# Kernel optimization log

Measured on AMD Instinct MI355X. Metric: run time of the kernel, lower is better.

## Reference

```python
import jax, jax.numpy as jnp
import numpy as np

IMG_DIM = 28 * 28


def _distmat(X):
    # D[i,j] = ||x_i||^2 - 2 x_i.x_j + ||x_j||^2
    r = jnp.sum(X * X, axis=1)
    a = X @ X.T
    return r[:, None] - 2.0 * a + r[None, :]


def _sigma_from_self(D, m):
    """Replicates sigma_estimation(X, X): median of the strict lower triangle of
    distmat(cat([X, X])), which is the 2x2 block-tiled matrix [[D,D],[D,D]].
    Its strict lower triangle multiset = full D (block 2,1) + 2x strict tril(D).
    Clamps: if med<=0 use mean; floor at 0.01. Detached (stop_gradient), matching
    the torch .detach().cpu().numpy() path."""
    mask = jnp.tril(jnp.ones((m, m), dtype=bool), -1)
    tril_inf = jnp.where(mask, D, jnp.inf)
    vals = jnp.concatenate([D.ravel(), tril_inf.ravel(), tril_inf.ravel()])
    s = jnp.sort(vals)  # inf padding sorts to the end
    k = 2 * m * m - m  # number of strict-lower-triangle entries of a 2m x 2m matrix
    if k % 2 == 0:
        med = 0.5 * (s[k // 2 - 1] + s[k // 2])  # np.median averages middles
    else:
        med = s[(k - 1) // 2]
    tri_sum = jnp.sum(jnp.where(mask, D, 0.0))
    mean_tri = (jnp.sum(D) + 2.0 * tri_sum) / k
    med = jnp.where(med <= 0.0, mean_tri, med)
    med = jnp.maximum(med, 0.01)
    return jax.lax.stop_gradient(med)


def _centered_kernel(D, sigma):
    # Kxc = Kx @ (I - ones/m)  ==  Kx - rowmean(Kx)
    K = jnp.exp(-D / (2.0 * sigma * sigma))
    return K - jnp.mean(K, axis=1, keepdims=True)


def _hsic_norm_from_kernels(Kxc, Kyc):
    Pxy = jnp.mean(Kxc * Kyc.T)
    Px = jnp.sqrt(jnp.mean(Kxc * Kxc.T))
    Py = jnp.sqrt(jnp.mean(Kyc * Kyc.T))
    return Pxy / (Px * Py)


def reference(x, y):
    x2 = x.reshape((-1, IMG_DIM))  # [m, 784]
    m = x2.shape[0]
    d = y.shape[-1]

    # hsic_normalized(x, y) with per-variable median sigma
    Dx = _distmat(x2)
    Dy = _distmat(y)
    Kx = _centered_kernel(Dx, _sigma_from_self(Dx, m))
    Ky = _centered_kernel(Dy, _sigma_from_self(Dy, m))
    mi_io = _hsic_norm_from_kernels(Kx, Ky)

    # Batched version of the nested loop over latent component pairs (i<j).
    # Per-column 1-D distance matrices: [d, m, m]
    yt = y.T  # [d, m]
    Dc = (yt[:, :, None] - yt[:, None, :]) ** 2
    sig = jax.vmap(lambda D: _sigma_from_self(D, m))(Dc)  # [d]
    Kc = jnp.exp(-Dc / (2.0 * sig * sig)[:, None, None])
    Kc = Kc - jnp.mean(Kc, axis=2, keepdims=True)  # centered, [d, m, m]

    # P[a,b] = mean(K_a * K_b^T)
    P = jnp.einsum('aij,bji->ab', Kc, Kc) / (m * m)
    diag = jnp.diagonal(P)
    norm = P / jnp.sqrt(diag[:, None] * diag[None, :])
    pair_mask = jnp.triu(jnp.ones((d, d), dtype=bool), 1)  # i < j
    mi_component_sum = jnp.sum(jnp.where(pair_mask, norm, 0.0))

    return -mi_io + mi_component_sum


def setup_inputs() -> dict:
    key = jax.random.key(0)
    kx, ky = jax.random.split(key)
    x = jax.random.normal(kx, (2048, 784), dtype=jnp.float32)
    y = jax.random.normal(ky, (2048, 10), dtype=jnp.float32)
    return {"x": x, "y": y}
```

## Files before the change

### kernel.cpp

```cpp
#include <hip/hip_runtime.h>
#include <math.h>

constexpr int Md   = 2048;
constexpr int NDIM = 784;
constexpr int DYC  = 10;
constexpr int MM   = Md * Md;
constexpr unsigned RANK_LO = 4193279u;
constexpr unsigned RANK_HI = 4193280u;
constexpr int NPROB = 12;
constexpr int NB    = 256;
constexpr int NBINS = 8192;

constexpr size_t OFF_DX     = 0;
constexpr size_t OFF_DY     = OFF_DX + (size_t)MM * 4;
constexpr size_t OFF_RX     = OFF_DY + (size_t)MM * 4;
constexpr size_t OFF_RY     = OFF_RX + Md * 8;
constexpr size_t OFF_RC     = OFF_RY + Md * 8;
constexpr size_t OFF_GACC   = OFF_RC + (size_t)DYC * Md * 8;
constexpr size_t OFF_HISTA  = OFF_GACC + 64 * 8;
constexpr size_t OFF_HISTB  = OFF_HISTA + (size_t)NPROB * NBINS * 4;
constexpr size_t OFF_RES    = OFF_HISTB + (size_t)NPROB * NBINS * 4;
constexpr size_t OFF_JOBS   = OFF_RES + 72 * 8;
constexpr size_t OFF_Q      = OFF_JOBS + NPROB * 5 * 4;
constexpr size_t OFF_RXN    = OFF_Q + NPROB * 4;
constexpr size_t OFF_YT     = OFF_RXN + Md * 4;
constexpr size_t WS_NEED    = OFF_YT + (size_t)DYC * Md * 4;
constexpr size_t ZERO_BASE  = OFF_GACC;
constexpr size_t ZERO_LEN   = OFF_JOBS - OFF_GACC;

typedef _Float16 f16x8 __attribute__((ext_vector_type(8)));
typedef _Float16 f16x4 __attribute__((ext_vector_type(4)));
typedef float    f32x16 __attribute__((ext_vector_type(16)));

__device__ __forceinline__ unsigned fkey(float v) {
  unsigned u = __float_as_uint(v);
  return (u & 0x80000000u) ? ~u : (u | 0x80000000u);
}
__device__ __forceinline__ float keyinv(unsigned k) {
  unsigned u = (k & 0x80000000u) ? (k ^ 0x80000000u) : ~k;
  return __uint_as_float(u);
}
__device__ __forceinline__ f16x8 ld8(const _Float16* p) {
  f16x4 lo = *(const f16x4*)p;
  f16x4 hi = *(const f16x4*)(p + 4);
  f16x8 r;
  r[0]=lo[0]; r[1]=lo[1]; r[2]=lo[2]; r[3]=lo[3];
  r[4]=hi[0]; r[5]=hi[1]; r[6]=hi[2]; r[7]=hi[3];
  return r;
}
__device__ __forceinline__ double waveReduceD(double v) {
  #pragma unroll
  for (int o = 32; o > 0; o >>= 1) v += __shfl_down(v, o, 64);
  return v;
}
__device__ __forceinline__ double blockReduceD(double v) {
  __shared__ double sred[4];
  v = waveReduceD(v);
  int lane = threadIdx.x & 63;
  int w    = threadIdx.x >> 6;
  __syncthreads();
  if (lane == 0) sred[w] = v;
  __syncthreads();
  double r = 0.0;
  if (threadIdx.x == 0) { r = sred[0] + sred[1] + sred[2] + sred[3]; }
  return r;
}

__global__ void fail_kernel(float* out) { if (threadIdx.x == 0) out[0] = 0.0f; }

__global__ __launch_bounds__(256) void prep_kernel(const float* __restrict__ X,
                                                   const float* __restrict__ Y,
                                                   float* __restrict__ rxn,
                                                   float* __restrict__ Yt,
                                                   unsigned* __restrict__ jobs) {
  int bb = blockIdx.x;
  if (bb < Md) {
    double acc = 0.0;
    for (int k = threadIdx.x; k < NDIM; k += 256) {
      float v = X[bb * NDIM + k];
      acc += (double)v * (double)v;
    }
    double r = blockReduceD(acc);
    if (threadIdx.x == 0) rxn[bb] = (float)r;
  } else if (bb < Md + 80) {
    int e = (bb - Md) * 256 + threadIdx.x;
    if (e < Md * DYC) {
      int i = e / DYC, c = e % DYC;
      Yt[c * Md + i] = Y[e];
    }
  } else {
    int t = threadIdx.x;
    if (t < NPROB * 5) {
      int w = t % 5;
      jobs[t] = (w == 1) ? RANK_LO : (w == 3) ? RANK_HI : 0u;
    }
  }
}

__global__ __launch_bounds__(256) void dist_kernel(const float* __restrict__ X,
                                                   const float* __restrict__ Y,
                                                   const float* __restrict__ rxn,
                                                   float* __restrict__ Dx,
                                                   float* __restrict__ Dy) {
  __shared__ _Float16 Ah[64][68], Al[64][68], Bh[64][68], Bl[64][68];
  __shared__ float Yi[64][10], Yj[64][10];
  const int tid = threadIdx.x;
  const int i0 = blockIdx.y * 64, j0 = blockIdx.x * 64;

  if (blockIdx.z == 1) {
    for (int t = tid; t < 640; t += 256) {
      int r = t / 10, c = t % 10;
      Yi[r][c] = Y[(i0 + r) * DYC + c];
      Yj[r][c] = Y[(j0 + r) * DYC + c];
    }
    __syncthreads();
    int jj = tid & 63;
    int ii0 = (tid >> 6) * 16;
    float yj[10];
    #pragma unroll
    for (int c = 0; c < 10; ++c) yj[c] = Yj[jj][c];
    for (int r = 0; r < 16; ++r) {
      int ii = ii0 + r;
      float s = 0.f;
      #pragma unroll
      for (int c = 0; c < 10; ++c) { float d = Yi[ii][c] - yj[c]; s = fmaf(d, d, s); }
      Dy[(size_t)(i0 + ii) * Md + (j0 + jj)] = s;
    }
    return;
  }

  const int wave = tid >> 6, lane = tid & 63;
  const int wr = (wave >> 1) * 32, wc = (wave & 1) * 32;
  const int srow = tid >> 2;
  const int sseg = (tid & 3) * 8;

  f32x16 acc_hh = {}, acc_c1 = {}, acc_c2 = {};

  const float* Arow = X + (size_t)(i0 + srow) * NDIM;
  const float* Brow = X + (size_t)(j0 + srow) * NDIM;
  const int lrow = lane & 31;
  const int lko  = (lane >> 5) * 8;

  for (int k0 = 0; k0 < 800; k0 += 32) {
    float a[8], b[8];
    if (k0 + 32 <= NDIM) {
      float4 a4 = *(const float4*)(Arow + k0 + sseg);
      float4 a5 = *(const float4*)(Arow + k0 + sseg + 4);
      float4 b4 = *(const float4*)(Brow + k0 + sseg);
      float4 b5 = *(const float4*)(Brow + k0 + sseg + 4);
      a[0]=a4.x; a[1]=a4.y; a[2]=a4.z; a[3]=a4.w; a[4]=a5.x; a[5]=a5.y; a[6]=a5.z; a[7]=a5.w;
      b[0]=b4.x; b[1]=b4.y; b[2]=b4.z; b[3]=b4.w; b[4]=b5.x; b[5]=b5.y; b[6]=b5.z; b[7]=b5.w;
    } else {
      #pragma unroll
      for (int u = 0; u < 8; ++u) {
        int k = k0 + sseg + u;
        a[u] = (k < NDIM) ? Arow[k] : 0.0f;
        b[u] = (k < NDIM) ? Brow[k] : 0.0f;
      }
    }
    __syncthreads();
    #pragma unroll
    for (int half = 0; half < 2; ++half) {
      f16x4 vah, val_, vbh, vbl;
      #pragma unroll
      for (int u = 0; u < 4; ++u) {
        float av = a[half * 4 + u];
        _Float16 h = (_Float16)av;
        vah[u] = h; val_[u] = (_Float16)(av - (float)h);
        float bv = b[half * 4 + u];
        _Float16 g = (_Float16)bv;
        vbh[u] = g; vbl[u] = (_Float16)(bv - (float)g);
      }
      *(f16x4*)&Ah[srow][sseg + half * 4] = vah;
      *(f16x4*)&Al[srow][sseg + half * 4] = val_;
      *(f16x4*)&Bh[srow][sseg + half * 4] = vbh;
      *(f16x4*)&Bl[srow][sseg + half * 4] = vbl;
    }
    __syncthreads();
    #pragma unroll
    for (int ks = 0; ks < 2; ++ks) {
      int ko = ks * 16 + lko;
      f16x8 fah = ld8(&Ah[wr + lrow][ko]);
      f16x8 fal = ld8(&Al[wr + lrow][ko]);
      f16x8 fbh = ld8(&Bh[wc + lrow][ko]);
      f16x8 fbl = ld8(&Bl[wc + lrow][ko]);
      acc_hh = __builtin_amdgcn_mfma_f32_32x32x16_f16(fah, fbh, acc_hh, 0, 0, 0);
      acc_c1 = __builtin_amdgcn_mfma_f32_32x32x16_f16(fah, fbl, acc_c1, 0, 0, 0);
      acc_c2 = __builtin_amdgcn_mfma_f32_32x32x16_f16(fal, fbh, acc_c2, 0, 0, 0);
    }
  }
  int col = j0 + wc + (lane & 31);
  float rj = rxn[col];
  #pragma unroll
  for (int r = 0; r < 16; ++r) {
    int row = i0 + wr + (r & 3) + 8 * (r >> 2) + 4 * (lane >> 5);
    float t = rxn[row] + rj;
    float cc = acc_c1[r] + acc_c2[r];
    Dx[(size_t)row * Md + col] = fmaf(-2.0f, cc, fmaf(-2.0f, acc_hh[r], t));
  }
}

__global__ __launch_bounds__(256) void hist_kernel(const float* __restrict__ Dx,
                                                   const float* __restrict__ Dy,
                                                   const float* __restrict__ Yt,
                                                   unsigned* __restrict__ histA,
                                                   unsigned* __restrict__ histB,
                                                   const unsigned* __restrict__ jobs,
                                                   int level) {
  __shared__ unsigned lh[NBINS];
  __shared__ float ycol[Md];
  int prob = blockIdx.y;
  for (int b = threadIdx.x; b < NBINS; b += 256) lh[b] = 0;
  const float* Mptr = (prob == 0) ? Dx : (prob == 1 ? Dy : nullptr);
  if (prob >= 2) {
    const float* src = Yt + (size_t)(prob - 2) * Md;
    for (int i = threadIdx.x; i < Md; i += 256) ycol[i] = src[i];
  }
  __syncthreads();
  unsigned pfxL = jobs[prob * 5 + 0];
  unsigned pfxH = jobs[prob * 5 + 2];
  unsigned div  = jobs[prob * 5 + 4];
  unsigned* ghB = histB + prob * NBINS;

  auto histo = [&](float v, unsigned w) {
    unsigned key = fkey(v);
    if (level == 0) {
      atomicAdd(&lh[key >> 19], w);
    } else if (level == 1) {
      if ((key >> 19) == pfxL)             atomicAdd(&lh[(key >> 6) & 8191u], w);
      else if (div && (key >> 19) == pfxH) atomicAdd(&ghB[(key >> 6) & 8191u], w);
    } else {
      if ((key >> 6) == pfxL)              atomicAdd(&lh[key & 63u], w);
      else if (div && (key >> 6) == pfxH)  atomicAdd(&ghB[key & 63u], w);
    }
  };

  for (int r = 0; r < Md / NB; ++r) {
    int i = blockIdx.x + r * NB;
    int n = i + 1, ng = n >> 2, tail = n & 3;
    if (Mptr) {
      const float4* row4 = (const float4*)(Mptr + (size_t)i * Md);
      for (int g = threadIdx.x; g < ng; g += 256) {
        float4 v = row4[g];
        int jb = g << 2;
        histo(v.x, (jb == i) ? 1u : 4u);
        histo(v.y, (jb + 1 == i) ? 1u : 4u);
        histo(v.z, (jb + 2 == i) ? 1u : 4u);
        histo(v.w, (jb + 3 == i) ? 1u : 4u);
      }
      if (threadIdx.x < tail) {
        int j = (ng << 2) + threadIdx.x;
        histo(Mptr[(size_t)i * Md + j], (j == i) ? 1u : 4u);
      }
    } else {
      float yi = ycol[i];
      for (int g = threadIdx.x; g < ng; g += 256) {
        float4 y4 = *(const float4*)&ycol[g << 2];
        int jb = g << 2;
        float d0 = yi - y4.x, d1 = yi - y4.y, d2 = yi - y4.z, d3 = yi - y4.w;
        histo(d0 * d0, (jb == i) ? 1u : 4u);
        histo(d1 * d1, (jb + 1 == i) ? 1u : 4u);
        histo(d2 * d2, (jb + 2 == i) ? 1u : 4u);
        histo(d3 * d3, (jb + 3 == i) ? 1u : 4u);
      }
      if (threadIdx.x < tail) {
        int j = (ng << 2) + threadIdx.x;
        float d = yi - ycol[j];
        histo(d * d, (j == i) ? 1u : 4u);
      }
    }
  }
  __syncthreads();
  unsigned* ghA = histA + prob * NBINS;
  for (int b = threadIdx.x; b < NBINS; b += 256) {
    unsigned v = lh[b];
    if (v) atomicAdd(&ghA[b], v);
  }
}

__global__ __launch_bounds__(256) void select_kernel(unsigned* __restrict__ histA,
                                                     unsigned* __restrict__ histB,
                                                     unsigned* __restrict__ jobs,
                                                     float* __restrict__ q,
                                                     int level) {
  __shared__ unsigned lhA[NBINS], lhB[NBINS];
  __shared__ unsigned psA[256], psB[256];
  int prob = blockIdx.x;
  int nbins = (level == 2) ? 64 : NBINS;
  int C = (nbins + 255) / 256;
  unsigned* ghA = histA + prob * NBINS;
  unsigned* ghB = histB + prob * NBINS;
  unsigned sA = 0, sB = 0;
  for (int k = 0; k < C; ++k) {
    int b = threadIdx.x * C + k;
    if (b < nbins) {
      unsigned v = ghA[b]; lhA[b] = v; sA += v;
      unsigned u = ghB[b]; lhB[b] = u; sB += u;
    }
  }
  psA[threadIdx.x] = sA; psB[threadIdx.x] = sB;
  __syncthreads();
  if (threadIdx.x == 0) {
    unsigned pfxL = jobs[prob * 5 + 0], remL = jobs[prob * 5 + 1];
    unsigned pfxH = jobs[prob * 5 + 2], remH = jobs[prob * 5 + 3];
    unsigned wasdiv = jobs[prob * 5 + 4];

    auto scan = [&](const unsigned* ps, const unsigned* lhp, unsigned r,
                    int& bin, unsigned& cum) {
      unsigned c = 0; int t = 0;
      for (; t < 255; ++t) { if (c + ps[t] > r) break; c += ps[t]; }
      int b = t * C;
      int be = b + C - 1; if (be > nbins - 1) be = nbins - 1;
      for (; b < be; ++b) { if (c + lhp[b] > r) break; c += lhp[b]; }
      bin = b; cum = c;
    };

    int bL; unsigned cL; scan(psA, lhA, remL, bL, cL);
    int bH; unsigned cH;
    unsigned div = wasdiv;
    if (!wasdiv) {
      scan(psA, lhA, remH, bH, cH);
      if (bH != bL) div = 1;
    } else {
      scan(psB, lhB, remH, bH, cH);
    }
    unsigned baseH = wasdiv ? pfxH : pfxL;
    if (level < 2) {
      jobs[prob * 5 + 0] = (level == 0) ? (unsigned)bL : ((pfxL << 13) | (unsigned)bL);
      jobs[prob * 5 + 2] = (level == 0) ? (unsigned)bH : ((baseH << 13) | (unsigned)bH);
      jobs[prob * 5 + 1] = remL - cL;
      jobs[prob * 5 + 3] = remH - cH;
      jobs[prob * 5 + 4] = div;
    } else {
      unsigned keyL = (pfxL << 6) | (unsigned)bL;
      unsigned keyH = (baseH << 6) | (unsigned)bH;
      float med = 0.5f * (keyinv(keyL) + keyinv(keyH));
      med = fmaxf(med, 0.01f);
      q[prob] = 2.0f * med * med;
    }
  }
  __syncthreads();
  for (int b = threadIdx.x; b < nbins; b += 256) { ghA[b] = 0; ghB[b] = 0; }
}

__global__ __launch_bounds__(256, 4) void phase3_kernel(const float* __restrict__ Dx,
                                                        const float* __restrict__ Dy,
                                                        const float* __restrict__ Yt,
                                                        const float* __restrict__ q,
                                                        double* __restrict__ Rx,
                                                        double* __restrict__ Ry,
                                                        double* __restrict__ Rc,
                                                        double* __restrict__ gacc) {
  __shared__ double shred[224];
  const int wave = threadIdx.x >> 6, lane = threadIdx.x & 63;
  int bb = blockIdx.x;

  if (bb < 256) {
    const float qx = q[0], qy = q[1];
    double gxx = 0, gxy = 0, gyy = 0;
    #pragma unroll
    for (int rr = 0; rr < 2; ++rr) {
      int i = bb * 4 + wave + rr * 1024;
      const float4* rx4 = (const float4*)(Dx + (size_t)i * Md);
      const float4* ry4 = (const float4*)(Dy + (size_t)i * Md);
      double ax = 0, ay = 0;
      #pragma unroll
      for (int it = 0; it < 8; ++it) {
        float4 xv = rx4[it * 64 + lane];
        float4 yv = ry4[it * 64 + lane];
        #pragma unroll
        for (int u = 0; u < 4; ++u) {
          float xe = (u == 0) ? xv.x : (u == 1) ? xv.y : (u == 2) ? xv.z : xv.w;
          float ye = (u == 0) ? yv.x : (u == 1) ? yv.y : (u == 2) ? yv.z : yv.w;
          float ex = expm1f(-(xe / qx));
          float ey = expm1f(-(ye / qy));
          ax += (double)ex; ay += (double)ey;
          gxx += (double)ex * ex;
          gxy += (double)ex * ey;
          gyy += (double)ey * ey;
        }
      }
      ax = waveReduceD(ax);
      ay = waveReduceD(ay);
      if (lane == 0) { Rx[i] = ax; Ry[i] = ay; }
    }
    gxx = waveReduceD(gxx);
    gxy = waveReduceD(gxy);
    gyy = waveReduceD(gyy);
    if (lane == 0) { shred[wave] = gxx; shred[4 + wave] = gxy; shred[8 + wave] = gyy; }
    __syncthreads();
    if (threadIdx.x == 0) {
      atomicAdd(&gacc[0], shred[0] + shred[1] + shred[2] + shred[3]);
      atomicAdd(&gacc[1], shred[4] + shred[5] + shred[6] + shred[7]);
      atomicAdd(&gacc[2], shred[8] + shred[9] + shred[10] + shred[11]);
    }
  } else if (bb < 768) {
    int i = (bb - 256) * 4 + wave;
    float yi[10], ninv[10];
    #pragma unroll
    for (int c = 0; c < 10; ++c) { yi[c] = Yt[c * Md + i]; ninv[c] = -1.0f / q[2 + c]; }
    float facc[10] = {};
    #pragma unroll 2
    for (int it = 0; it < 8; ++it) {
      int j = it * 256 + lane * 4;
      #pragma unroll
      for (int c = 0; c < 10; ++c) {
        float4 v = *(const float4*)(Yt + c * Md + j);
        float d0 = yi[c] - v.x, d1 = yi[c] - v.y, d2 = yi[c] - v.z, d3 = yi[c] - v.w;
        facc[c] += __expf(d0 * d0 * ninv[c]) - 1.0f;
        facc[c] += __expf(d1 * d1 * ninv[c]) - 1.0f;
        facc[c] += __expf(d2 * d2 * ninv[c]) - 1.0f;
        facc[c] += __expf(d3 * d3 * ninv[c]) - 1.0f;
      }
    }
    #pragma unroll
    for (int c = 0; c < 10; ++c) {
      double r = waveReduceD((double)facc[c]);
      if (lane == 0) Rc[c * Md + i] = r;
    }
  } else {
    float ninv[10];
    #pragma unroll
    for (int c = 0; c < 10; ++c) ninv[c] = -1.0f / q[2 + c];
    int tid0 = (bb - 768) * 256 + threadIdx.x;
    int j = tid0 & 2047;
    float yj[10];
    #pragma unroll
    for (int c = 0; c < 10; ++c) yj[c] = Yt[c * Md + j];
    float facc[55];
    #pragma unroll
    for (int k = 0; k < 55; ++k) facc[k] = 0.0f;
    for (int i = tid0 >> 11; i < Md; i += 64) {
      float e[10];
      #pragma unroll
      for (int c = 0; c < 10; ++c) {
        float d = Yt[c * Md + i] - yj[c];
        e[c] = __expf(d * d * ninv[c]) - 1.0f;
      }
      int k = 0;
      #pragma unroll
      for (int a = 0; a < 10; ++a)
        #pragma unroll
        for (int b = a; b < 10; ++b) { facc[k] = fmaf(e[a], e[b], facc[k]); ++k; }
    }
    #pragma unroll
    for (int k = 0; k < 55; ++k) {
      double v = waveReduceD((double)facc[k]);
      if (lane == 0) shred[k * 4 + wave] = v;
    }
    __syncthreads();
    for (int k = threadIdx.x; k < 55; k += 256) {
      double v = shred[k * 4] + shred[k * 4 + 1] + shred[k * 4 + 2] + shred[k * 4 + 3];
      atomicAdd(&gacc[3 + k], v);
    }
  }
}

__global__ __launch_bounds__(256) void final_sums_kernel(const double* __restrict__ Rx,
                                                         const double* __restrict__ Ry,
                                                         const double* __restrict__ Rc,
                                                         double* __restrict__ res) {
  int k = blockIdx.x;
  double acc = 0.0;
  if (k < 5) {
    for (int i = threadIdx.x; i < Md; i += 256) {
      double a = Rx[i], b = Ry[i];
      acc += (k == 0) ? a : (k == 1) ? b : (k == 2) ? a * b : (k == 3) ? a * a : b * b;
    }
  } else if (k < 15) {
    const double* p = Rc + (size_t)(k - 5) * Md;
    for (int i = threadIdx.x; i < Md; i += 256) acc += p[i];
  } else {
    int kk = k - 15;
    int a = 0;
    while (kk >= 10 - a) { kk -= 10 - a; ++a; }
    int b = a + kk;
    const double* pa = Rc + (size_t)a * Md;
    const double* pb = Rc + (size_t)b * Md;
    for (int i = threadIdx.x; i < Md; i += 256) acc += pa[i] * pb[i];
  }
  double r = blockReduceD(acc);
  if (threadIdx.x == 0) res[k] = r;
}

__global__ void final_combine_kernel(const double* __restrict__ res,
                                     const double* __restrict__ gacc,
                                     float* __restrict__ out) {
  if (threadIdx.x != 0) return;
  const double m = (double)Md, m2 = m * m;
  double Gxx = gacc[0], Gxy = gacc[1], Gyy = gacc[2];
  double Sxy = Gxy - (2.0 / m) * res[2] + (res[0] * res[1]) / m2;
  double Sxx = Gxx - (2.0 / m) * res[3] + (res[0] * res[0]) / m2;
  double Syy = Gyy - (2.0 / m) * res[4] + (res[1] * res[1]) / m2;
  double mi_io = Sxy / sqrt(Sxx * Syy);

  double Sc[55], diag[10];
  int k = 0;
  for (int a = 0; a < 10; ++a)
    for (int b = a; b < 10; ++b) {
      double S = gacc[3 + k] - (2.0 / m) * res[15 + k] + (res[5 + a] * res[5 + b]) / m2;
      Sc[k] = S;
      if (a == b) diag[a] = S;
      ++k;
    }
  double comp = 0.0;
  k = 0;
  for (int a = 0; a < 10; ++a)
    for (int b = a; b < 10; ++b) {
      if (b > a) comp += Sc[k] / sqrt(diag[a] * diag[b]);
      ++k;
    }
  out[0] = (float)(-mi_io + comp);
}

extern "C" void kernel_launch(void* const* d_in, const int* in_sizes, int n_in,
                              void* d_out, int out_size, void* d_ws, size_t ws_size,
                              hipStream_t stream) {
  const float* X = (const float*)d_in[0];
  const float* Y = (const float*)d_in[1];
  float* out = (float*)d_out;
  char* ws = (char*)d_ws;

  if (ws_size < WS_NEED) {
    fail_kernel<<<1, 64, 0, stream>>>(out);
    return;
  }

  float*    Dx    = (float*)(ws + OFF_DX);
  float*    Dy    = (float*)(ws + OFF_DY);
  double*   Rx    = (double*)(ws + OFF_RX);
  double*   Ry    = (double*)(ws + OFF_RY);
  double*   Rc    = (double*)(ws + OFF_RC);
  double*   gacc  = (double*)(ws + OFF_GACC);
  unsigned* histA = (unsigned*)(ws + OFF_HISTA);
  unsigned* histB = (unsigned*)(ws + OFF_HISTB);
  double*   res   = (double*)(ws + OFF_RES);
  unsigned* jobs  = (unsigned*)(ws + OFF_JOBS);
  float*    q     = (float*)(ws + OFF_Q);
  float*    rxn   = (float*)(ws + OFF_RXN);
  float*    Yt    = (float*)(ws + OFF_YT);

  hipMemsetAsync(ws + ZERO_BASE, 0, ZERO_LEN, stream);
  prep_kernel<<<Md + 80 + 1, 256, 0, stream>>>(X, Y, rxn, Yt, jobs);
  dist_kernel<<<dim3(32, 32, 2), 256, 0, stream>>>(X, Y, rxn, Dx, Dy);

  for (int lvl = 0; lvl < 3; ++lvl) {
    hist_kernel<<<dim3(NB, NPROB), 256, 0, stream>>>(Dx, Dy, Yt, histA, histB, jobs, lvl);
    select_kernel<<<NPROB, 256, 0, stream>>>(histA, histB, jobs, q, lvl);
  }

  phase3_kernel<<<1280, 256, 0, stream>>>(Dx, Dy, Yt, q, Rx, Ry, Rc, gacc);
  final_sums_kernel<<<70, 256, 0, stream>>>(Rx, Ry, Rc, res);
  final_combine_kernel<<<1, 64, 0, stream>>>(res, gacc, out);
}
```

Measured before the change: 443.0 us.

## Compute only lower-triangular distance tiles and split phase3 into two kernels

The distance kernel now launches only the 528 lower-triangular 64x64 tiles, derives tile coordinates from a triangular index, and mirrors each result into the transposed position. This roughly halves the MFMA work for Dx. The cost is strided transposed stores, which are uncoalesced. The component-pair grand-sum branch of phase3 is moved into its own kernel, which gives each part its own register budget and launch bounds.

Result: faster. 428.5 us (-3.3%).

```diff
diff --git a/kernel.cpp b/kernel.cpp
--- a/kernel.cpp
+++ b/kernel.cpp
@@ -10,6 +10,7 @@
 constexpr int NPROB = 12;
 constexpr int NB    = 256;
 constexpr int NBINS = 8192;
+constexpr int NTRI  = 528;
 
 constexpr size_t OFF_DX     = 0;
 constexpr size_t OFF_DY     = OFF_DX + (size_t)MM * 4;
@@ -105,7 +106,13 @@
   __shared__ _Float16 Ah[64][68], Al[64][68], Bh[64][68], Bl[64][68];
   __shared__ float Yi[64][10], Yj[64][10];
   const int tid = threadIdx.x;
-  const int i0 = blockIdx.y * 64, j0 = blockIdx.x * 64;
+  int t0 = blockIdx.x;
+  int bi = (int)((sqrtf(8.0f * (float)t0 + 1.0f) - 1.0f) * 0.5f);
+  while ((bi + 1) * (bi + 2) / 2 <= t0) ++bi;
+  while (bi * (bi + 1) / 2 > t0) --bi;
+  int bj = t0 - bi * (bi + 1) / 2;
+  const int i0 = bi * 64, j0 = bj * 64;
+  const bool offdiag = (bi != bj);
 
   if (blockIdx.z == 1) {
     for (int t = tid; t < 640; t += 256) {
@@ -125,6 +132,7 @@
       #pragma unroll
       for (int c = 0; c < 10; ++c) { float d = Yi[ii][c] - yj[c]; s = fmaf(d, d, s); }
       Dy[(size_t)(i0 + ii) * Md + (j0 + jj)] = s;
+      if (offdiag) Dy[(size_t)(j0 + jj) * Md + (i0 + ii)] = s;
     }
     return;
   }
@@ -196,7 +204,9 @@
     int row = i0 + wr + (r & 3) + 8 * (r >> 2) + 4 * (lane >> 5);
     float t = rxn[row] + rj;
     float cc = acc_c1[r] + acc_c2[r];
-    Dx[(size_t)row * Md + col] = fmaf(-2.0f, cc, fmaf(-2.0f, acc_hh[r], t));
+    float v = fmaf(-2.0f, cc, fmaf(-2.0f, acc_hh[r], t));
+    Dx[(size_t)row * Md + col] = v;
+    if (offdiag) Dx[(size_t)col * Md + row] = v;
   }
 }
 
@@ -343,15 +353,15 @@
   for (int b = threadIdx.x; b < nbins; b += 256) { ghA[b] = 0; ghB[b] = 0; }
 }
 
-__global__ __launch_bounds__(256, 4) void phase3_kernel(const float* __restrict__ Dx,
-                                                        const float* __restrict__ Dy,
-                                                        const float* __restrict__ Yt,
-                                                        const float* __restrict__ q,
-                                                        double* __restrict__ Rx,
-                                                        double* __restrict__ Ry,
-                                                        double* __restrict__ Rc,
-                                                        double* __restrict__ gacc) {
-  __shared__ double shred[224];
+__global__ __launch_bounds__(256) void phase3a_kernel(const float* __restrict__ Dx,
+                                                      const float* __restrict__ Dy,
+                                                      const float* __restrict__ Yt,
+                                                      const float* __restrict__ q,
+                                                      double* __restrict__ Rx,
+                                                      double* __restrict__ Ry,
+                                                      double* __restrict__ Rc,
+                                                      double* __restrict__ gacc) {
+  __shared__ double shred[12];
   const int wave = threadIdx.x >> 6, lane = threadIdx.x & 63;
   int bb = blockIdx.x;
 
@@ -394,7 +404,7 @@
       atomicAdd(&gacc[1], shred[4] + shred[5] + shred[6] + shred[7]);
       atomicAdd(&gacc[2], shred[8] + shred[9] + shred[10] + shred[11]);
     }
-  } else if (bb < 768) {
+  } else {
     int i = (bb - 256) * 4 + wave;
     float yi[10], ninv[10];
     #pragma unroll
@@ -418,41 +428,47 @@
       double r = waveReduceD((double)facc[c]);
       if (lane == 0) Rc[c * Md + i] = r;
     }
-  } else {
-    float ninv[10];
-    #pragma unroll
-    for (int c = 0; c < 10; ++c) ninv[c] = -1.0f / q[2 + c];
-    int tid0 = (bb - 768) * 256 + threadIdx.x;
-    int j = tid0 & 2047;
-    float yj[10];
-    #pragma unroll
-    for (int c = 0; c < 10; ++c) yj[c] = Yt[c * Md + j];
-    float facc[55];
-    #pragma unroll
-    for (int k = 0; k < 55; ++k) facc[k] = 0.0f;
-    for (int i = tid0 >> 11; i < Md; i += 64) {
-      float e[10];
+  }
+}
+
+__global__ __launch_bounds__(256) void comp_grand_kernel(const float* __restrict__ Yt,
+                                                         const float* __restrict__ q,
+                                                         double* __restrict__ gacc) {
+  __shared__ double shred[220];
+  const int wave = threadIdx.x >> 6, lane = threadIdx.x & 63;
+  float ninv[10];
+  #pragma unroll
+  for (int c = 0; c < 10; ++c) ninv[c] = -1.0f / q[2 + c];
+  int tid0 = blockIdx.x * 256 + threadIdx.x;
+  int j = tid0 & 2047;
+  float yj[10];
+  #pragma unroll
+  for (int c = 0; c < 10; ++c) yj[c] = Yt[c * Md + j];
+  float facc[55];
+  #pragma unroll
+  for (int k = 0; k < 55; ++k) facc[k] = 0.0f;
+  for (int i = tid0 >> 11; i < Md; i += 64) {
+    float e[10];
+    #pragma unroll
+    for (int c = 0; c < 10; ++c) {
+      float d = Yt[c * Md + i] - yj[c];
+      e[c] = __expf(d * d * ninv[c]) - 1.0f;
+    }
+    int k = 0;
+    #pragma unroll
+    for (int a = 0; a < 10; ++a)
       #pragma unroll
-      for (int c = 0; c < 10; ++c) {
-        float d = Yt[c * Md + i] - yj[c];
-        e[c] = __expf(d * d * ninv[c]) - 1.0f;
-      }
-      int k = 0;
-      #pragma unroll
-      for (int a = 0; a < 10; ++a)
-        #pragma unroll
-        for (int b = a; b < 10; ++b) { facc[k] = fmaf(e[a], e[b], facc[k]); ++k; }
-    }
-    #pragma unroll
-    for (int k = 0; k < 55; ++k) {
-      double v = waveReduceD((double)facc[k]);
-      if (lane == 0) shred[k * 4 + wave] = v;
-    }
-    __syncthreads();
-    for (int k = threadIdx.x; k < 55; k += 256) {
-      double v = shred[k * 4] + shred[k * 4 + 1] + shred[k * 4 + 2] + shred[k * 4 + 3];
-      atomicAdd(&gacc[3 + k], v);
-    }
+      for (int b = a; b < 10; ++b) { facc[k] = fmaf(e[a], e[b], facc[k]); ++k; }
+  }
+  #pragma unroll
+  for (int k = 0; k < 55; ++k) {
+    double v = waveReduceD((double)facc[k]);
+    if (lane == 0) shred[k * 4 + wave] = v;
+  }
+  __syncthreads();
+  for (int k = threadIdx.x; k < 55; k += 256) {
+    double v = shred[k * 4] + shred[k * 4 + 1] + shred[k * 4 + 2] + shred[k * 4 + 3];
+    atomicAdd(&gacc[3 + k], v);
   }
 }
 
@@ -542,14 +558,15 @@
 
   hipMemsetAsync(ws + ZERO_BASE, 0, ZERO_LEN, stream);
   prep_kernel<<<Md + 80 + 1, 256, 0, stream>>>(X, Y, rxn, Yt, jobs);
-  dist_kernel<<<dim3(32, 32, 2), 256, 0, stream>>>(X, Y, rxn, Dx, Dy);
+  dist_kernel<<<dim3(NTRI, 1, 2), 256, 0, stream>>>(X, Y, rxn, Dx, Dy);
 
   for (int lvl = 0; lvl < 3; ++lvl) {
     hist_kernel<<<dim3(NB, NPROB), 256, 0, stream>>>(Dx, Dy, Yt, histA, histB, jobs, lvl);
     select_kernel<<<NPROB, 256, 0, stream>>>(histA, histB, jobs, q, lvl);
   }
 
-  phase3_kernel<<<1280, 256, 0, stream>>>(Dx, Dy, Yt, q, Rx, Ry, Rc, gacc);
+  phase3a_kernel<<<768, 256, 0, stream>>>(Dx, Dy, Yt, q, Rx, Ry, Rc, gacc);
+  comp_grand_kernel<<<512, 256, 0, stream>>>(Yt, q, gacc);
   final_sums_kernel<<<70, 256, 0, stream>>>(Rx, Ry, Rc, res);
   final_combine_kernel<<<1, 64, 0, stream>>>(res, gacc, out);
 }
```
